# Kernel optimization log

Hardware: AMD Instinct MI355X
Metric: run time of the kernel (lower is better)

Reference implementation:

```python
import jax, jax.numpy as jnp
import numpy as np

N_HEAD = 16


def setup_inputs() -> dict:
    key = jax.random.key(0)
    ks = jax.random.split(key, 10)
    N, C, P = 4096, 2048, 8
    s = lambda k, shape, scale: jax.random.normal(k, shape, dtype=jnp.float32) * scale
    return {
        "x": s(ks[0], (N, C), 1.0),
        "rwkv_state": s(ks[1], (N, C), 1.0),
        "Wq": s(ks[2], (C, C), C ** -0.5),
        "Wk": s(ks[3], (C, C), C ** -0.5),
        "Wv": s(ks[4], (C, C), C ** -0.5),
        "Wo": s(ks[5], (C, C), 0.1 * C ** -0.5),
        "Wg": s(ks[6], (C, C), C ** -0.5),
        "bg": jnp.zeros((C,), dtype=jnp.float32),
        "Wb": s(ks[7], (2 * C, P * C), (2 * C) ** -0.5),
        "Wr": s(ks[8], (C, C), C ** -0.5),
    }


def reference(x, rwkv_state, Wq, Wk, Wv, Wo, Wg, bg, Wb, Wr):
    N, C = x.shape
    H = N_HEAD
    D = C // H
    # bridge: produce per-token tiny prefix [N, P, C] + reconstruction loss
    xs = jnp.concatenate([x, rwkv_state], axis=-1)      # [N, 2C]
    prefix = (xs @ Wb).reshape(N, -1, C)                # [N, P, C]
    recon = prefix.mean(axis=1) @ Wr                    # [N, C]
    recon_loss = jnp.mean((recon - x) ** 2)
    # per-token attention: query length 1 over P prefix keys
    q = (x @ Wq).reshape(N, H, D)                       # [N, H, D]
    k = (prefix @ Wk).reshape(N, -1, H, D)              # [N, P, H, D]
    v = (prefix @ Wv).reshape(N, -1, H, D)
    scores = jnp.einsum('nhd,nphd->nhp', q, k) / jnp.sqrt(jnp.float32(D))
    attn = jax.nn.softmax(scores, axis=-1)              # [N, H, P]
    out = jnp.einsum('nhp,nphd->nhd', attn, v).reshape(N, C)
    g = jax.nn.sigmoid(x @ Wg + bg)
    out = (out @ Wo) * g
    return out, recon_loss
```

## Files before the change

### kernel.cpp

```cpp
#include <hip/hip_runtime.h>

#define DEVFN static __device__ __forceinline__

typedef __attribute__((ext_vector_type(8))) short short8;
typedef __attribute__((ext_vector_type(4))) float f32x4;

DEVFN unsigned short f2bf(float f) {
    union { float f; unsigned u; } a; a.f = f;
    unsigned u = a.u;
    unsigned r = (u + 0x7FFFu + ((u >> 16) & 1u)) >> 16;
    return (unsigned short)r;
}
DEVFN float bf2f(unsigned short b) {
    union { unsigned u; float f; } a; a.u = ((unsigned)b) << 16;
    return a.f;
}
DEVFN float2 bfpair(unsigned v) {
    float2 r;
    union { unsigned u; float f; } a;
    a.u = (v & 0xFFFFu) << 16; r.x = a.f;
    a.u = v & 0xFFFF0000u;     r.y = a.f;
    return r;
}

DEVFN void gload16(const void* g, void* lds) {
    __builtin_amdgcn_global_load_lds(
        (const __attribute__((address_space(1))) unsigned int*)g,
        (__attribute__((address_space(3))) unsigned int*)lds, 16, 0, 0);
}

#define BAR() __builtin_amdgcn_s_barrier()
#define VMCNT4() asm volatile("s_waitcnt vmcnt(4)" ::: "memory")
#define VMCNT0() asm volatile("s_waitcnt vmcnt(0)" ::: "memory")

DEVFN void pack_xs_body(const float* __restrict__ x, const float* __restrict__ r,
                        unsigned short* __restrict__ xs, int blk) {
    int i = blk * 256 + threadIdx.x;
    int n  = i >> 10;
    int cw = i & 1023;
    const float* src = (cw < 512) ? (x + (size_t)n * 2048 + cw * 4)
                                  : (r + (size_t)n * 2048 + (cw - 512) * 4);
    float4 v = *(const float4*)src;
    ushort4 o;
    o.x = f2bf(v.x); o.y = f2bf(v.y); o.z = f2bf(v.z); o.w = f2bf(v.w);
    *(ushort4*)(xs + (size_t)n * 4096 + cw * 4) = o;
}

DEVFN void transpose_body(const float* __restrict__ in,
                          unsigned short* __restrict__ out,
                          int R, int Cc, int bx, int by) {
    __shared__ float tile[32][33];
    const int t  = threadIdx.x;
    const int r  = t >> 3;
    const int c4 = (t & 7) * 4;
    const int tr = by * 32, tc = bx * 32;
    float4 v = *(const float4*)(in + (size_t)(tr + r) * Cc + tc + c4);
    tile[r][c4 + 0] = v.x; tile[r][c4 + 1] = v.y;
    tile[r][c4 + 2] = v.z; tile[r][c4 + 3] = v.w;
    __syncthreads();
    const int orow = r, oc = c4;
    ushort4 o;
    o.x = f2bf(tile[oc + 0][orow]);
    o.y = f2bf(tile[oc + 1][orow]);
    o.z = f2bf(tile[oc + 2][orow]);
    o.w = f2bf(tile[oc + 3][orow]);
    *(ushort4*)(out + (size_t)(tc + orow) * R + tr + oc) = o;
}

__global__ __launch_bounds__(256) void prep_kernel(
        const float* __restrict__ x, const float* __restrict__ rwkv,
        unsigned short* __restrict__ xs,
        const float* __restrict__ Wb, unsigned short* __restrict__ wbT,
        const float* __restrict__ i0, const float* __restrict__ i1,
        const float* __restrict__ i2, const float* __restrict__ i3,
        const float* __restrict__ i4, const float* __restrict__ i5,
        unsigned short* __restrict__ o0, unsigned short* __restrict__ o1,
        unsigned short* __restrict__ o2, unsigned short* __restrict__ o3,
        unsigned short* __restrict__ o4, unsigned short* __restrict__ o5) {
    int b = blockIdx.x;
    if (b < 16384) { pack_xs_body(x, rwkv, xs, b); return; }
    b -= 16384;
    if (b < 65536) { transpose_body(Wb, wbT, 4096, 16384, b & 511, b >> 9); return; }
    b -= 65536;
    const int z = b >> 12, rem = b & 4095;
    const float* in; unsigned short* out;
    switch (z) {
        case 0: in = i0; out = o0; break;
        case 1: in = i1; out = o1; break;
        case 2: in = i2; out = o2; break;
        case 3: in = i3; out = o3; break;
        case 4: in = i4; out = o4; break;
        default: in = i5; out = o5; break;
    }
    transpose_body(in, out, 2048, 2048, rem & 63, rem >> 6);
}

template <int EPI>
__global__ __launch_bounds__(512, 2) void gemm256(
        const unsigned short* __restrict__ A, int lda,
        const unsigned short* __restrict__ Bt, int ldb,
        void* __restrict__ Cptr, void* __restrict__ Cptr2,
        int ldc, int splitcol, int K, int Mtiles,
        const float* __restrict__ aux_f32,
        const unsigned short* __restrict__ aux_bf16,
        float* __restrict__ loss_accum,
        const unsigned short* __restrict__ A2,
        const unsigned short* __restrict__ Bt2) {
    extern __shared__ char smem[];
    const int tid  = threadIdx.x;
    const int wid  = tid >> 6, lane = tid & 63;
    const int wm   = wid >> 2, wn = wid & 3;
    const int l15  = lane & 15;
    const int lhi  = (lane >> 4) * 16;
    const int nkt  = K >> 6;

    int bid = blockIdx.x;
    bool sub1 = false;
    if constexpr (EPI == 5) {
        const int half = gridDim.x >> 1;
        if (bid >= half) { sub1 = true; bid -= half; A = A2; Bt = Bt2; }
    }

    const int bandH = Mtiles >> 3;
    const int xcd = bid & 7, idx = bid >> 3;
    const int brow = (xcd * bandH + (idx % bandH)) << 8;
    const int bcol = (idx / bandH) << 8;

    const int lin0 = (wid * 2 + 0) * 1024 + lane * 16;
    const int lin1 = (wid * 2 + 1) * 1024 + lane * 16;
    const int ph0 = lin0 ^ (((lin0 >> 7) & 7) << 4);
    const int ph1v = lin1 ^ (((lin1 >> 7) & 7) << 4);
    const int srow0 = ph0 >> 7, scol0 = (ph0 & 127) >> 1;
    const int srow1 = ph1v >> 7, scol1 = (ph1v & 127) >> 1;
    const int dst0 = (wid * 2 + 0) * 1024;
    const int dst1 = (wid * 2 + 1) * 1024;

#define STAGE(t, mat, h) do { \
        char* base_ = smem + (((t) & 1) * 65536) + ((mat) * 32768) + ((h) * 16384); \
        const unsigned short* G_ = (mat) ? Bt : A; \
        const int ld_ = (mat) ? ldb : lda; \
        const int rb_ = ((mat) ? bcol : brow) + (h) * 128; \
        gload16(G_ + (size_t)(rb_ + srow0) * ld_ + (t) * 64 + scol0, base_ + dst0); \
        gload16(G_ + (size_t)(rb_ + srow1) * ld_ + (t) * 64 + scol1, base_ + dst1); \
    } while (0)
#define STAGE_G(t, mat, h) do { if ((t) < nkt) STAGE(t, mat, h); } while (0)

#define LDA_FRAG(dst, buf, m, kk) do { \
        int lin_ = ((m) * 16 + l15) * 128 + (kk) * 64 + lhi; \
        int ph_  = lin_ ^ (((lin_ >> 7) & 7) << 4); \
        dst = *(const short8*)(smem + (buf) * 65536 + wm * 16384 + ph_); \
    } while (0)
#define LDB_FRAG(dst, buf, n, kk) do { \
        int lin_ = ((wn & 1) * 64 + (n) * 16 + l15) * 128 + (kk) * 64 + lhi; \
        int ph_  = lin_ ^ (((lin_ >> 7) & 7) << 4); \
        dst = *(const short8*)(smem + (buf) * 65536 + 32768 + (wn >> 1) * 16384 + ph_); \
    } while (0)

    f32x4 acc[8][4] = {};
    short8 afr[8][2], bfr[4][2];

#define MFMA_Q(mq) do { \
        __builtin_amdgcn_s_setprio(1); \
        _Pragma("unroll") \
        for (int n_ = 0; n_ < 4; ++n_) { \
            acc[2*(mq)][n_]   = __builtin_amdgcn_mfma_f32_16x16x32_bf16(afr[2*(mq)][0],   bfr[n_][0], acc[2*(mq)][n_],   0,0,0); \
            acc[2*(mq)][n_]   = __builtin_amdgcn_mfma_f32_16x16x32_bf16(afr[2*(mq)][1],   bfr[n_][1], acc[2*(mq)][n_],   0,0,0); \
            acc[2*(mq)+1][n_] = __builtin_amdgcn_mfma_f32_16x16x32_bf16(afr[2*(mq)+1][0], bfr[n_][0], acc[2*(mq)+1][n_], 0,0,0); \
            acc[2*(mq)+1][n_] = __builtin_amdgcn_mfma_f32_16x16x32_bf16(afr[2*(mq)+1][1], bfr[n_][1], acc[2*(mq)+1][n_], 0,0,0); \
        } \
        __builtin_amdgcn_s_setprio(0); \
    } while (0)

#define READ_B(b) do { \
        _Pragma("unroll") \
        for (int n_ = 0; n_ < 4; ++n_) { LDB_FRAG(bfr[n_][0], b, n_, 0); LDB_FRAG(bfr[n_][1], b, n_, 1); } \
    } while (0)
#define READ_QA(b, mq) do { \
        LDA_FRAG(afr[2*(mq)][0],   b, 2*(mq),   0); LDA_FRAG(afr[2*(mq)][1],   b, 2*(mq),   1); \
        LDA_FRAG(afr[2*(mq)+1][0], b, 2*(mq)+1, 0); LDA_FRAG(afr[2*(mq)+1][1], b, 2*(mq)+1, 1); \
    } while (0)

    STAGE(0, 1, 0); STAGE(0, 1, 1); STAGE(0, 0, 0); STAGE(0, 0, 1);
    STAGE_G(1, 1, 0); STAGE_G(1, 1, 1);
    VMCNT4();
    BAR();

    const int niter = nkt >> 1;
    for (int it = 0; it < niter; ++it) {
        const int t0 = it * 2, t1 = t0 + 1;
        const bool lastIt = (it == niter - 1);

        READ_B(0); READ_QA(0, 0); READ_QA(0, 1);
        STAGE_G(t1, 0, 0); STAGE_G(t1, 0, 1);
        BAR();
        MFMA_Q(0); MFMA_Q(1);
        READ_QA(0, 2); READ_QA(0, 3);
        STAGE_G(t0 + 2, 1, 0); STAGE_G(t0 + 2, 1, 1);
        if (lastIt) { VMCNT0(); } else { VMCNT4(); }
        BAR();
        MFMA_Q(2); MFMA_Q(3);
        READ_B(1); READ_QA(1, 0); READ_QA(1, 1);
        STAGE_G(t0 + 2, 0, 0); STAGE_G(t0 + 2, 0, 1);
        BAR();
        MFMA_Q(0); MFMA_Q(1);
        READ_QA(1, 2); READ_QA(1, 3);
        STAGE_G(t1 + 2, 1, 0); STAGE_G(t1 + 2, 1, 1);
        if (lastIt) { VMCNT0(); } else { VMCNT4(); }
        BAR();
        MFMA_Q(2); MFMA_Q(3);
    }

    const int rl = (lane >> 4) * 4;
    const int cl = lane & 15;
    const int row0 = brow + wm * 128;

    if constexpr (EPI == 5) {
        const int col0 = bcol + wn * 64;
        if (!sub1) {
            float lsum = 0.f;
#pragma unroll
            for (int m = 0; m < 8; m++)
#pragma unroll
                for (int n = 0; n < 4; n++)
#pragma unroll
                    for (int rg = 0; rg < 4; rg++) {
                        int gr = row0 + m * 16 + rl + rg;
                        int gc = col0 + n * 16 + cl;
                        float d = acc[m][n][rg] - aux_f32[(size_t)gr * ldc + gc];
                        lsum += d * d;
                    }
#pragma unroll
            for (int msk = 1; msk < 64; msk <<= 1)
                lsum += __shfl_xor(lsum, msk, 64);
            if (lane == 0) atomicAdd(loss_accum, lsum);
        } else {
#pragma unroll
            for (int m = 0; m < 8; m++)
#pragma unroll
                for (int n = 0; n < 4; n++)
#pragma unroll
                    for (int rg = 0; rg < 4; rg++) {
                        int gr = row0 + m * 16 + rl + rg;
                        int gc = col0 + n * 16 + cl;
                        size_t idxo = (size_t)gr * ldc + gc;
                        float gv = bf2f(aux_bf16[idxo]);
                        ((float*)Cptr)[idxo] = acc[m][n][rg] * gv;
                    }
        }
        return;
    }

    void* Ceff = Cptr;
    bool second = false;
    int bcol_l = bcol;
    if constexpr (EPI == 0 || EPI == 4) {
        if (bcol >= splitcol) { Ceff = Cptr2; bcol_l = bcol - splitcol; second = true; }
    }
    const int col0 = bcol_l + wn * 64;

#pragma unroll
    for (int m = 0; m < 8; m++)
#pragma unroll
        for (int n = 0; n < 4; n++)
#pragma unroll
            for (int rg = 0; rg < 4; rg++) {
                int gr = row0 + m * 16 + rl + rg;
                int gc = col0 + n * 16 + cl;
                size_t idxo = (size_t)gr * ldc + gc;
                if constexpr (EPI == 0) {
                    ((unsigned short*)Ceff)[idxo] = f2bf(acc[m][n][rg]);
                } else {
                    if (second) {
                        float t = acc[m][n][rg] + aux_f32[gc];
                        ((unsigned short*)Ceff)[idxo] = f2bf(1.f / (1.f + expf(-t)));
                    } else {
                        ((unsigned short*)Ceff)[idxo] = f2bf(acc[m][n][rg]);
                    }
                }
            }
#undef STAGE
#undef STAGE_G
#undef LDA_FRAG
#undef LDB_FRAG
#undef MFMA_Q
#undef READ_B
#undef READ_QA
}

__global__ __launch_bounds__(256) void pmean_kernel(
        const unsigned short* __restrict__ prefix, unsigned short* __restrict__ pm) {
    int i  = blockIdx.x * 256 + threadIdx.x;
    int n  = i >> 8;
    int c8 = (i & 255) * 8;
    float acc[8] = {0, 0, 0, 0, 0, 0, 0, 0};
#pragma unroll
    for (int p = 0; p < 8; p++) {
        const unsigned short* src = prefix + (size_t)n * 16384 + p * 2048 + c8;
        uint4 raw = *(const uint4*)src;
        unsigned w[4] = {raw.x, raw.y, raw.z, raw.w};
#pragma unroll
        for (int j = 0; j < 4; j++) {
            float2 fp = bfpair(w[j]);
            acc[2 * j] += fp.x; acc[2 * j + 1] += fp.y;
        }
    }
    uint4 o;
    unsigned* ow = (unsigned*)&o;
#pragma unroll
    for (int j = 0; j < 4; j++)
        ow[j] = (unsigned)f2bf(acc[2 * j] * 0.125f) |
                ((unsigned)f2bf(acc[2 * j + 1] * 0.125f) << 16);
    *(uint4*)(pm + (size_t)n * 2048 + c8) = o;
}

__global__ __launch_bounds__(256) void attn_kernel(
        const unsigned short* __restrict__ q, const unsigned short* __restrict__ k,
        const unsigned short* __restrict__ v, unsigned short* __restrict__ o) {
    int gw   = (blockIdx.x * 256 + threadIdx.x) >> 6;
    int lane = threadIdx.x & 63;
    int n = gw >> 4, h = gw & 15;
    size_t qoff = (size_t)n * 2048 + h * 128 + lane * 2;
    float2 qv = bfpair(*(const unsigned*)(q + qoff));
    float s[8];
#pragma unroll
    for (int p = 0; p < 8; p++) {
        size_t koff = (size_t)(n * 8 + p) * 2048 + h * 128 + lane * 2;
        float2 kv = bfpair(*(const unsigned*)(k + koff));
        float d = qv.x * kv.x + qv.y * kv.y;
#pragma unroll
        for (int msk = 1; msk < 64; msk <<= 1) d += __shfl_xor(d, msk, 64);
        s[p] = d * 0.08838834764831845f;
    }
    float mx = s[0];
#pragma unroll
    for (int p = 1; p < 8; p++) mx = fmaxf(mx, s[p]);
    float e[8], den = 0.f;
#pragma unroll
    for (int p = 0; p < 8; p++) { e[p] = expf(s[p] - mx); den += e[p]; }
    float inv = 1.f / den;
    float o0 = 0.f, o1 = 0.f;
#pragma unroll
    for (int p = 0; p < 8; p++) {
        size_t voff = (size_t)(n * 8 + p) * 2048 + h * 128 + lane * 2;
        float2 vv = bfpair(*(const unsigned*)(v + voff));
        float a = e[p] * inv;
        o0 += a * vv.x; o1 += a * vv.y;
    }
    *(unsigned*)(o + qoff) = (unsigned)f2bf(o0) | ((unsigned)f2bf(o1) << 16);
}

__global__ __launch_bounds__(64) void finalize_loss_kernel(
        const float* __restrict__ accum, float* __restrict__ dst) {
    if (threadIdx.x == 0) dst[0] = accum[0] * (1.0f / (4096.0f * 2048.0f));
}

extern "C" void kernel_launch(void* const* d_in, const int* in_sizes, int n_in,
                              void* d_out, int out_size, void* d_ws, size_t ws_size,
                              hipStream_t stream) {
    const float* x    = (const float*)d_in[0];
    const float* rwkv = (const float*)d_in[1];
    const float* Wq   = (const float*)d_in[2];
    const float* Wk   = (const float*)d_in[3];
    const float* Wv   = (const float*)d_in[4];
    const float* Wo   = (const float*)d_in[5];
    const float* Wg   = (const float*)d_in[6];
    const float* bg   = (const float*)d_in[7];
    const float* Wb   = (const float*)d_in[8];
    const float* Wr   = (const float*)d_in[9];
    float* out = (float*)d_out;
    char*  ws  = (char*)d_ws;

    unsigned short* xs     = (unsigned short*)(ws + 0ull);
    unsigned short* wbT    = (unsigned short*)(ws + 33554432ull);
    unsigned short* wqT    = (unsigned short*)(ws + 167772160ull);
    unsigned short* wgT    = (unsigned short*)(ws + 176160768ull);
    unsigned short* wkT    = (unsigned short*)(ws + 184549376ull);
    unsigned short* wvT    = (unsigned short*)(ws + 192937984ull);
    unsigned short* wrT    = (unsigned short*)(ws + 201326592ull);
    unsigned short* woT    = (unsigned short*)(ws + 209715200ull);
    unsigned short* prefix = (unsigned short*)(ws + 218103808ull);
    unsigned short* vbuf   = (unsigned short*)(ws + 352321536ull);
    unsigned short* qbuf   = (unsigned short*)(ws + 486539264ull);
    unsigned short* gbuf   = (unsigned short*)(ws + 503316480ull);
    unsigned short* pmean  = (unsigned short*)(ws + 520093696ull);
    unsigned short* attno  = (unsigned short*)(ws + 536870912ull);
    float*          lossA  = (float*)(ws + 553648128ull);
    unsigned short* kbuf   = wbT;

    const int SMEM = 131072;
    const int BIG = 1 << 30;
    hipFuncSetAttribute(reinterpret_cast<const void*>(gemm256<0>),
                        hipFuncAttributeMaxDynamicSharedMemorySize, SMEM);
    hipFuncSetAttribute(reinterpret_cast<const void*>(gemm256<4>),
                        hipFuncAttributeMaxDynamicSharedMemorySize, SMEM);
    hipFuncSetAttribute(reinterpret_cast<const void*>(gemm256<5>),
                        hipFuncAttributeMaxDynamicSharedMemorySize, SMEM);

    hipMemsetAsync(lossA, 0, 16, stream);

    prep_kernel<<<106496, 256, 0, stream>>>(
        x, rwkv, xs, Wb, wbT,
        Wq, Wg, Wk, Wv, Wr, Wo, wqT, wgT, wkT, wvT, wrT, woT);

    gemm256<0><<<dim3(1024), 512, SMEM, stream>>>(xs, 4096, wbT, 4096,
        prefix, nullptr, 16384, BIG, 4096, 16, nullptr, nullptr, nullptr,
        nullptr, nullptr);
    gemm256<0><<<dim3(2048), 512, SMEM, stream>>>(prefix, 2048, wkT, 2048,
        kbuf, vbuf, 2048, 2048, 2048, 128, nullptr, nullptr, nullptr,
        nullptr, nullptr);
    pmean_kernel<<<4096, 256, 0, stream>>>(prefix, pmean);
    gemm256<4><<<dim3(256), 512, SMEM, stream>>>(xs, 4096, wqT, 2048,
        qbuf, gbuf, 2048, 2048, 2048, 16, bg, nullptr, nullptr,
        nullptr, nullptr);
    attn_kernel<<<16384, 256, 0, stream>>>(qbuf, kbuf, vbuf, attno);
    gemm256<5><<<dim3(256), 512, SMEM, stream>>>(pmean, 2048, wrT, 2048,
        out, nullptr, 2048, BIG, 2048, 16, x, gbuf, lossA,
        attno, woT);

    finalize_loss_kernel<<<1, 64, 0, stream>>>(lossA, out + 8388608);
}
```

Baseline: 1.267 ms.

## Reassociate attention to avoid projecting prefix through Wk and Wv

Instead of computing K = prefix@Wk and V = prefix@Wv for all N*P rows, the query is first projected per head through Wk^T (q_h @ Wk_h^T giving a C-wide vector per head). Scores are then dot products against the raw prefix, the attention-weighted prefix sum is formed per head, and that sum is multiplied by the per-head Wv slice. This drops the large N*P x C x 2C GEMM in favour of an N x C x C*H-sized GEMM, a per-token LDS attention kernel and a per-head Wv GEMM. The cost is large per-head intermediate buffers (16 x N x C bf16) and a simple, non-pipelined Wv GEMM kernel.

```diff
diff --git a/kernel.cpp b/kernel.cpp
--- a/kernel.cpp
+++ b/kernel.cpp
@@ -14,13 +14,6 @@
 DEVFN float bf2f(unsigned short b) {
     union { unsigned u; float f; } a; a.u = ((unsigned)b) << 16;
     return a.f;
-}
-DEVFN float2 bfpair(unsigned v) {
-    float2 r;
-    union { unsigned u; float f; } a;
-    a.u = (v & 0xFFFFu) << 16; r.x = a.f;
-    a.u = v & 0xFFFF0000u;     r.y = a.f;
-    return r;
 }
 
 DEVFN void gload16(const void* g, void* lds) {
@@ -67,30 +60,40 @@
     *(ushort4*)(out + (size_t)(tc + orow) * R + tr + oc) = o;
 }
 
+DEVFN void cast_body(const float* __restrict__ in,
+                     unsigned short* __restrict__ out, int blk) {
+    int i = blk * 1024 + threadIdx.x * 4;
+    float4 v = *(const float4*)(in + i);
+    ushort4 o;
+    o.x = f2bf(v.x); o.y = f2bf(v.y); o.z = f2bf(v.z); o.w = f2bf(v.w);
+    *(ushort4*)(out + i) = o;
+}
+
 __global__ __launch_bounds__(256) void prep_kernel(
         const float* __restrict__ x, const float* __restrict__ rwkv,
         unsigned short* __restrict__ xs,
         const float* __restrict__ Wb, unsigned short* __restrict__ wbT,
         const float* __restrict__ i0, const float* __restrict__ i1,
         const float* __restrict__ i2, const float* __restrict__ i3,
-        const float* __restrict__ i4, const float* __restrict__ i5,
+        const float* __restrict__ i4,
         unsigned short* __restrict__ o0, unsigned short* __restrict__ o1,
         unsigned short* __restrict__ o2, unsigned short* __restrict__ o3,
-        unsigned short* __restrict__ o4, unsigned short* __restrict__ o5) {
+        unsigned short* __restrict__ o4,
+        const float* __restrict__ Wk, unsigned short* __restrict__ wkC) {
     int b = blockIdx.x;
     if (b < 16384) { pack_xs_body(x, rwkv, xs, b); return; }
     b -= 16384;
     if (b < 65536) { transpose_body(Wb, wbT, 4096, 16384, b & 511, b >> 9); return; }
     b -= 65536;
     const int z = b >> 12, rem = b & 4095;
+    if (z == 5) { cast_body(Wk, wkC, rem); return; }
     const float* in; unsigned short* out;
     switch (z) {
         case 0: in = i0; out = o0; break;
         case 1: in = i1; out = o1; break;
         case 2: in = i2; out = o2; break;
         case 3: in = i3; out = o3; break;
-        case 4: in = i4; out = o4; break;
-        default: in = i5; out = o5; break;
+        default: in = i4; out = o4; break;
     }
     transpose_body(in, out, 2048, 2048, rem & 63, rem >> 6);
 }
@@ -116,9 +119,17 @@
 
     int bid = blockIdx.x;
     bool sub1 = false;
+    unsigned short* Cq = nullptr;
     if constexpr (EPI == 5) {
         const int half = gridDim.x >> 1;
         if (bid >= half) { sub1 = true; bid -= half; A = A2; Bt = Bt2; }
+    }
+    if constexpr (EPI == 6) {
+        const int h = bid & 15; bid >>= 4;
+        A  += h * 128;
+        Bt += h * 128;
+        Cq = (h < 8) ? (unsigned short*)Cptr  + (size_t)h * 8388608
+                     : (unsigned short*)Cptr2 + (size_t)(h - 8) * 8388608;
     }
 
     const int bandH = Mtiles >> 3;
@@ -135,15 +146,15 @@
     const int dst0 = (wid * 2 + 0) * 1024;
     const int dst1 = (wid * 2 + 1) * 1024;
 
-#define STAGE(t, mat, h) do { \
-        char* base_ = smem + (((t) & 1) * 65536) + ((mat) * 32768) + ((h) * 16384); \
+#define STAGE(t, mat, h_) do { \
+        char* base_ = smem + (((t) & 1) * 65536) + ((mat) * 32768) + ((h_) * 16384); \
         const unsigned short* G_ = (mat) ? Bt : A; \
         const int ld_ = (mat) ? ldb : lda; \
-        const int rb_ = ((mat) ? bcol : brow) + (h) * 128; \
+        const int rb_ = ((mat) ? bcol : brow) + (h_) * 128; \
         gload16(G_ + (size_t)(rb_ + srow0) * ld_ + (t) * 64 + scol0, base_ + dst0); \
         gload16(G_ + (size_t)(rb_ + srow1) * ld_ + (t) * 64 + scol1, base_ + dst1); \
     } while (0)
-#define STAGE_G(t, mat, h) do { if ((t) < nkt) STAGE(t, mat, h); } while (0)
+#define STAGE_G(t, mat, h_) do { if ((t) < nkt) STAGE(t, mat, h_); } while (0)
 
 #define LDA_FRAG(dst, buf, m, kk) do { \
         int lin_ = ((m) * 16 + l15) * 128 + (kk) * 64 + lhi; \
@@ -214,6 +225,21 @@
     const int cl = lane & 15;
     const int row0 = brow + wm * 128;
 
+    if constexpr (EPI == 6) {
+        const int col0 = bcol + wn * 64;
+#pragma unroll
+        for (int m = 0; m < 8; m++)
+#pragma unroll
+            for (int n = 0; n < 4; n++)
+#pragma unroll
+                for (int rg = 0; rg < 4; rg++) {
+                    int gr = row0 + m * 16 + rl + rg;
+                    int gc = col0 + n * 16 + cl;
+                    Cq[(size_t)gr * 2048 + gc] = f2bf(acc[m][n][rg]);
+                }
+        return;
+    }
+
     if constexpr (EPI == 5) {
         const int col0 = bcol + wn * 64;
         if (!sub1) {
@@ -300,8 +326,8 @@
         unsigned w[4] = {raw.x, raw.y, raw.z, raw.w};
 #pragma unroll
         for (int j = 0; j < 4; j++) {
-            float2 fp = bfpair(w[j]);
-            acc[2 * j] += fp.x; acc[2 * j + 1] += fp.y;
+            acc[2 * j]     += bf2f((unsigned short)(w[j] & 0xFFFFu));
+            acc[2 * j + 1] += bf2f((unsigned short)(w[j] >> 16));
         }
     }
     uint4 o;
@@ -313,40 +339,138 @@
     *(uint4*)(pm + (size_t)n * 2048 + c8) = o;
 }
 
-__global__ __launch_bounds__(256) void attn_kernel(
-        const unsigned short* __restrict__ q, const unsigned short* __restrict__ k,
-        const unsigned short* __restrict__ v, unsigned short* __restrict__ o) {
-    int gw   = (blockIdx.x * 256 + threadIdx.x) >> 6;
-    int lane = threadIdx.x & 63;
-    int n = gw >> 4, h = gw & 15;
-    size_t qoff = (size_t)n * 2048 + h * 128 + lane * 2;
-    float2 qv = bfpair(*(const unsigned*)(q + qoff));
-    float s[8];
-#pragma unroll
-    for (int p = 0; p < 8; p++) {
-        size_t koff = (size_t)(n * 8 + p) * 2048 + h * 128 + lane * 2;
-        float2 kv = bfpair(*(const unsigned*)(k + koff));
-        float d = qv.x * kv.x + qv.y * kv.y;
-#pragma unroll
-        for (int msk = 1; msk < 64; msk <<= 1) d += __shfl_xor(d, msk, 64);
-        s[p] = d * 0.08838834764831845f;
-    }
-    float mx = s[0];
-#pragma unroll
-    for (int p = 1; p < 8; p++) mx = fmaxf(mx, s[p]);
-    float e[8], den = 0.f;
-#pragma unroll
-    for (int p = 0; p < 8; p++) { e[p] = expf(s[p] - mx); den += e[p]; }
-    float inv = 1.f / den;
-    float o0 = 0.f, o1 = 0.f;
-#pragma unroll
-    for (int p = 0; p < 8; p++) {
-        size_t voff = (size_t)(n * 8 + p) * 2048 + h * 128 + lane * 2;
-        float2 vv = bfpair(*(const unsigned*)(v + voff));
-        float a = e[p] * inv;
-        o0 += a * vv.x; o1 += a * vv.y;
-    }
-    *(unsigned*)(o + qoff) = (unsigned)f2bf(o0) | ((unsigned)f2bf(o1) << 16);
+__global__ __launch_bounds__(256) void attn2_kernel(
+        const unsigned short* __restrict__ prefix,
+        unsigned short* __restrict__ qtA, unsigned short* __restrict__ qtB) {
+    __shared__ __align__(16) unsigned short pfx[8][2048];
+    const int n = blockIdx.x, tid = threadIdx.x;
+    const int wid = tid >> 6, lane = tid & 63;
+#pragma unroll
+    for (int r = 0; r < 8; ++r)
+        *(uint4*)&pfx[r][tid * 8] =
+            *(const uint4*)(prefix + (size_t)n * 16384 + r * 2048 + tid * 8);
+    __syncthreads();
+#pragma unroll
+    for (int hh = 0; hh < 4; ++hh) {
+        const int h = wid * 4 + hh;
+        unsigned short* qrow = ((h < 8) ? qtA + (size_t)h * 8388608
+                                        : qtB + (size_t)(h - 8) * 8388608)
+                               + (size_t)n * 2048;
+        short8 qv[4];
+#pragma unroll
+        for (int k = 0; k < 4; ++k)
+            qv[k] = *(const short8*)(qrow + lane * 8 + k * 512);
+        float s[8];
+#pragma unroll
+        for (int p = 0; p < 8; ++p) {
+            float d = 0.f;
+#pragma unroll
+            for (int k = 0; k < 4; ++k) {
+                short8 pv = *(const short8*)&pfx[p][lane * 8 + k * 512];
+#pragma unroll
+                for (int j = 0; j < 8; ++j)
+                    d += bf2f((unsigned short)qv[k][j]) * bf2f((unsigned short)pv[j]);
+            }
+#pragma unroll
+            for (int msk = 1; msk < 64; msk <<= 1) d += __shfl_xor(d, msk, 64);
+            s[p] = d * 0.08838834764831845f;
+        }
+        float mx = s[0];
+#pragma unroll
+        for (int p = 1; p < 8; ++p) mx = fmaxf(mx, s[p]);
+        float e[8], den = 0.f;
+#pragma unroll
+        for (int p = 0; p < 8; ++p) { e[p] = expf(s[p] - mx); den += e[p]; }
+        float inv = 1.f / den;
+#pragma unroll
+        for (int k = 0; k < 4; ++k) {
+            float wa[8] = {0, 0, 0, 0, 0, 0, 0, 0};
+#pragma unroll
+            for (int p = 0; p < 8; ++p) {
+                float a = e[p] * inv;
+                short8 pv = *(const short8*)&pfx[p][lane * 8 + k * 512];
+#pragma unroll
+                for (int j = 0; j < 8; ++j)
+                    wa[j] += a * bf2f((unsigned short)pv[j]);
+            }
+            short8 ov;
+#pragma unroll
+            for (int j = 0; j < 8; ++j) ov[j] = (short)f2bf(wa[j]);
+            *(short8*)(qrow + lane * 8 + k * 512) = ov;
+        }
+    }
+}
+
+__global__ __launch_bounds__(512) void gemmwv_kernel(
+        const unsigned short* __restrict__ qtA,
+        const unsigned short* __restrict__ qtB,
+        const unsigned short* __restrict__ wvT,
+        unsigned short* __restrict__ attno) {
+    __shared__ __align__(16) unsigned short Atile[256 * 64];
+    __shared__ __align__(16) unsigned short Btile[128 * 64];
+    const int tid = threadIdx.x, wid = tid >> 6, lane = tid & 63;
+    const int wm = wid >> 1, wn = wid & 1;
+    const int l15 = lane & 15, lhi = (lane >> 4) * 16;
+    const int h = blockIdx.x >> 4, mt = blockIdx.x & 15;
+    const unsigned short* A = (h < 8) ? qtA + (size_t)h * 8388608
+                                      : qtB + (size_t)(h - 8) * 8388608;
+    const unsigned short* B = wvT + (size_t)(h * 128) * 2048;
+    const int brow = mt << 8;
+
+#define WVST(buf, c, kt, G, ld, rbase) do { \
+        int linc = (c) * 8192 + wid * 1024 + lane * 16; \
+        int phc = linc ^ (((linc >> 7) & 7) << 4); \
+        gload16((G) + (size_t)((rbase) + (phc >> 7)) * (ld) + (kt) * 64 + ((phc & 127) >> 1), \
+                (char*)(buf) + (c) * 8192 + wid * 1024); \
+    } while (0)
+
+    f32x4 acc[4][4] = {};
+    for (int kt = 0; kt < 32; ++kt) {
+        WVST(Atile, 0, kt, A, 2048, brow); WVST(Atile, 1, kt, A, 2048, brow);
+        WVST(Atile, 2, kt, A, 2048, brow); WVST(Atile, 3, kt, A, 2048, brow);
+        WVST(Btile, 0, kt, B, 2048, 0);    WVST(Btile, 1, kt, B, 2048, 0);
+        VMCNT0();
+        BAR();
+        short8 af[4][2], bf[4][2];
+#pragma unroll
+        for (int m = 0; m < 4; ++m)
+#pragma unroll
+            for (int kk = 0; kk < 2; ++kk) {
+                int lin = (wm * 64 + m * 16 + l15) * 128 + kk * 64 + lhi;
+                int ph = lin ^ (((lin >> 7) & 7) << 4);
+                af[m][kk] = *(const short8*)((char*)Atile + ph);
+            }
+#pragma unroll
+        for (int nn = 0; nn < 4; ++nn)
+#pragma unroll
+            for (int kk = 0; kk < 2; ++kk) {
+                int lin = (wn * 64 + nn * 16 + l15) * 128 + kk * 64 + lhi;
+                int ph = lin ^ (((lin >> 7) & 7) << 4);
+                bf[nn][kk] = *(const short8*)((char*)Btile + ph);
+            }
+        __builtin_amdgcn_s_setprio(1);
+#pragma unroll
+        for (int m = 0; m < 4; ++m)
+#pragma unroll
+            for (int nn = 0; nn < 4; ++nn) {
+                acc[m][nn] = __builtin_amdgcn_mfma_f32_16x16x32_bf16(af[m][0], bf[nn][0], acc[m][nn], 0, 0, 0);
+                acc[m][nn] = __builtin_amdgcn_mfma_f32_16x16x32_bf16(af[m][1], bf[nn][1], acc[m][nn], 0, 0, 0);
+            }
+        __builtin_amdgcn_s_setprio(0);
+        BAR();
+    }
+    const int rl = (lane >> 4) * 4, cl = lane & 15;
+#pragma unroll
+    for (int m = 0; m < 4; ++m)
+#pragma unroll
+        for (int nn = 0; nn < 4; ++nn)
+#pragma unroll
+            for (int rg = 0; rg < 4; ++rg) {
+                int gr = brow + wm * 64 + m * 16 + rl + rg;
+                int gc = h * 128 + wn * 64 + nn * 16 + cl;
+                attno[(size_t)gr * 2048 + gc] = f2bf(acc[m][nn][rg]);
+            }
+#undef WVST
 }
 
 __global__ __launch_bounds__(64) void finalize_loss_kernel(
@@ -372,20 +496,20 @@
 
     unsigned short* xs     = (unsigned short*)(ws + 0ull);
     unsigned short* wbT    = (unsigned short*)(ws + 33554432ull);
+    unsigned short* qtA    = (unsigned short*)(ws + 33554432ull);
     unsigned short* wqT    = (unsigned short*)(ws + 167772160ull);
     unsigned short* wgT    = (unsigned short*)(ws + 176160768ull);
-    unsigned short* wkT    = (unsigned short*)(ws + 184549376ull);
+    unsigned short* wkC    = (unsigned short*)(ws + 184549376ull);
     unsigned short* wvT    = (unsigned short*)(ws + 192937984ull);
     unsigned short* wrT    = (unsigned short*)(ws + 201326592ull);
     unsigned short* woT    = (unsigned short*)(ws + 209715200ull);
     unsigned short* prefix = (unsigned short*)(ws + 218103808ull);
-    unsigned short* vbuf   = (unsigned short*)(ws + 352321536ull);
+    unsigned short* qtB    = (unsigned short*)(ws + 352321536ull);
     unsigned short* qbuf   = (unsigned short*)(ws + 486539264ull);
     unsigned short* gbuf   = (unsigned short*)(ws + 503316480ull);
     unsigned short* pmean  = (unsigned short*)(ws + 520093696ull);
     unsigned short* attno  = (unsigned short*)(ws + 536870912ull);
     float*          lossA  = (float*)(ws + 553648128ull);
-    unsigned short* kbuf   = wbT;
 
     const int SMEM = 131072;
     const int BIG = 1 << 30;
@@ -395,24 +519,27 @@
                         hipFuncAttributeMaxDynamicSharedMemorySize, SMEM);
     hipFuncSetAttribute(reinterpret_cast<const void*>(gemm256<5>),
                         hipFuncAttributeMaxDynamicSharedMemorySize, SMEM);
+    hipFuncSetAttribute(reinterpret_cast<const void*>(gemm256<6>),
+                        hipFuncAttributeMaxDynamicSharedMemorySize, SMEM);
 
     hipMemsetAsync(lossA, 0, 16, stream);
 
     prep_kernel<<<106496, 256, 0, stream>>>(
         x, rwkv, xs, Wb, wbT,
-        Wq, Wg, Wk, Wv, Wr, Wo, wqT, wgT, wkT, wvT, wrT, woT);
+        Wq, Wg, Wv, Wr, Wo, wqT, wgT, wvT, wrT, woT, Wk, wkC);
 
     gemm256<0><<<dim3(1024), 512, SMEM, stream>>>(xs, 4096, wbT, 4096,
         prefix, nullptr, 16384, BIG, 4096, 16, nullptr, nullptr, nullptr,
-        nullptr, nullptr);
-    gemm256<0><<<dim3(2048), 512, SMEM, stream>>>(prefix, 2048, wkT, 2048,
-        kbuf, vbuf, 2048, 2048, 2048, 128, nullptr, nullptr, nullptr,
         nullptr, nullptr);
     pmean_kernel<<<4096, 256, 0, stream>>>(prefix, pmean);
     gemm256<4><<<dim3(256), 512, SMEM, stream>>>(xs, 4096, wqT, 2048,
         qbuf, gbuf, 2048, 2048, 2048, 16, bg, nullptr, nullptr,
         nullptr, nullptr);
-    attn_kernel<<<16384, 256, 0, stream>>>(qbuf, kbuf, vbuf, attno);
+    gemm256<6><<<dim3(2048), 512, SMEM, stream>>>(qbuf, 2048, wkC, 2048,
+        qtA, qtB, 2048, BIG, 128, 16, nullptr, nullptr, nullptr,
+        nullptr, nullptr);
+    attn2_kernel<<<4096, 256, 0, stream>>>(prefix, qtA, qtB);
+    gemmwv_kernel<<<256, 512, 0, stream>>>(qtA, qtB, wvT, attno);
     gemm256<5><<<dim3(256), 512, SMEM, stream>>>(pmean, 2048, wrT, 2048,
         out, nullptr, 2048, BIG, 2048, 16, x, gbuf, lossA,
         attno, woT);
```

After: 1.095 ms. -13.6%, faster.
